# Kernel optimization log

Measured on AMD Instinct MI355X. Metric: run time of the kernel, lower is better.

## Reference

```python
import jax, jax.numpy as jnp
import numpy as np

INPUT_SIZE = 1024
HIDDEN_SIZE = 2048
BATCH = 8192


def setup_inputs() -> dict:
    key = jax.random.key(0)
    k1, k2, k3, k4, k5 = jax.random.split(key, 5)
    input_tensor = jax.random.normal(k1, (BATCH, INPUT_SIZE), dtype=jnp.float32)
    h_0 = jax.random.normal(k2, (BATCH, HIDDEN_SIZE), dtype=jnp.float32)
    c_0 = jax.random.normal(k3, (BATCH, HIDDEN_SIZE), dtype=jnp.float32)
    # parameters: weight [input_size, 3*hidden], weight_hidden [hidden, 3*hidden], bias [3*hidden]
    weight = jax.random.normal(k4, (INPUT_SIZE, 3 * HIDDEN_SIZE), dtype=jnp.float32) * 0.02
    weight_hidden = jax.random.normal(k5, (HIDDEN_SIZE, 3 * HIDDEN_SIZE), dtype=jnp.float32) * 0.02
    bias = jnp.zeros((3 * HIDDEN_SIZE,), dtype=jnp.float32)
    return {
        "input_tensor": input_tensor,
        "h_0": h_0,
        "c_0": c_0,
        "weight": weight,
        "weight_hidden": weight_hidden,
        "bias": bias,
    }


def reference(input_tensor, h_0, c_0, weight, weight_hidden, bias):
    hidden_size = h_0.shape[-1]
    # pre-activations: x @ W + h_0 @ W_h + b  -> [batch, 3*hidden]
    gates = input_tensor @ weight + h_0 @ weight_hidden + bias
    f, i, c = jnp.split(gates, 3, axis=1)
    # c_1 = sigmoid(f) * c_0 + sigmoid(i) * tanh(c)
    c_1 = jax.nn.sigmoid(f) * c_0 + jax.nn.sigmoid(i) * jnp.tanh(c)
    return c_1
```

## Files before the change

### kernel.cpp

```cpp
#include <hip/hip_runtime.h>
#include <stdint.h>


#define BATCH 8192
#define INSZ  1024
#define HID   2048
#define NG    6144
#define KTOT  3072
#define KTILES 96

typedef __attribute__((ext_vector_type(8))) short short8;
typedef __attribute__((ext_vector_type(4))) short short4v;
typedef __attribute__((ext_vector_type(4))) float f32x4;
typedef __attribute__((ext_vector_type(4))) unsigned short u16x4;

__device__ __forceinline__ unsigned short f32_to_bf16(float f) {
  uint32_t u = __builtin_bit_cast(uint32_t, f);
  u += 0x7fffu + ((u >> 16) & 1u);
  return (unsigned short)(u >> 16);
}


__global__ __launch_bounds__(256) void pack_a_kernel(
    const float* __restrict__ x, const float* __restrict__ h,
    unsigned short* __restrict__ Ap) {
  uint32_t q   = blockIdx.x * 256u + threadIdx.x;
  uint32_t kk4 = q & 7u;
  uint32_t m   = (q >> 3) & 8191u;
  uint32_t kt  = q >> 16;
  uint32_t k   = kt * 32u + kk4 * 4u;
  const float* src = (k < INSZ) ? (x + (size_t)m * INSZ + k)
                                : (h + (size_t)m * HID + (k - INSZ));
  float4 v = *(const float4*)src;
  u16x4 o;
  o.x = f32_to_bf16(v.x); o.y = f32_to_bf16(v.y);
  o.z = f32_to_bf16(v.z); o.w = f32_to_bf16(v.w);
  uint32_t c  = kk4 >> 1, hh = kk4 & 1;
  uint32_t sm = (m + (m >> 2)) & 3u;
  *(u16x4*)(Ap + ((size_t)kt * BATCH + m) * 32 + ((c ^ sm) * 8 + hh * 4)) = o;
}

__global__ __launch_bounds__(256) void pack_b_kernel(
    const float* __restrict__ W, const float* __restrict__ Wh,
    unsigned short* __restrict__ Bp) {
  uint32_t q  = blockIdx.x * 256u + threadIdx.x;
  uint32_t hh = q & 7u;
  uint32_t r  = q >> 3;
  uint32_t n  = r % 6144u;
  uint32_t kt = r / 6144u;
  uint32_t k0 = kt * 32u + hh * 4u;
  float v[4];
#pragma unroll
  for (int t = 0; t < 4; ++t) {
    uint32_t k = k0 + t;
    v[t] = (k < INSZ) ? W[(size_t)k * NG + n]
                      : Wh[(size_t)(k - INSZ) * NG + n];
  }
  u16x4 o;
  o.x = f32_to_bf16(v[0]); o.y = f32_to_bf16(v[1]);
  o.z = f32_to_bf16(v[2]); o.w = f32_to_bf16(v[3]);
  *(u16x4*)(Bp + ((size_t)kt * NG + n) * 32 + hh * 4) = o;
}

__device__ __forceinline__ void lstm_epilogue(
    const f32x4 acc[4][6], int m0, int j0, int wm, int wn, int quad, int l16,
    const float* __restrict__ bias, const float* __restrict__ c0,
    float* __restrict__ out) {
#pragma unroll
  for (int mi = 0; mi < 4; ++mi) {
    int rowb = m0 + wm * 64 + mi * 16 + quad * 4;
#pragma unroll
    for (int p = 0; p < 2; ++p) {
      int j = j0 + (2 * wn + p) * 16 + l16;
      float bfv = bias[j], biv = bias[HID + j], bcv = bias[2 * HID + j];
#pragma unroll
      for (int r = 0; r < 4; ++r) {
        size_t idx = (size_t)(rowb + r) * HID + j;
        float fg = acc[mi][0 + p][r] + bfv;
        float ig = acc[mi][2 + p][r] + biv;
        float cg = acc[mi][4 + p][r] + bcv;
        float sf = 1.f / (1.f + __expf(-fg));
        float si = 1.f / (1.f + __expf(-ig));
        float th = 2.f / (1.f + __expf(-2.f * cg)) - 1.f;
        out[idx] = sf * c0[idx] + si * th;
      }
    }
  }
}

__global__ __launch_bounds__(256) void gemm_packed_kernel(
    const unsigned short* __restrict__ Ap, const unsigned short* __restrict__ Bp,
    const float* __restrict__ bias, const float* __restrict__ c0,
    float* __restrict__ out) {
  __shared__ __align__(16) unsigned short As[128 * 32];
  const int tid = threadIdx.x;
  const int lane = tid & 63, w = tid >> 6;
  const int wm = w >> 1, wn = w & 1;
  const int quad = lane >> 4, l16 = lane & 15;
  const int bx = blockIdx.x;
  const int mt = bx & 63, jt = bx >> 6;
  const int m0 = mt * 128, j0 = jt * 64;
  const int sw = (l16 + (l16 >> 2)) & 3;

  f32x4 acc[4][6];
#pragma unroll
  for (int a = 0; a < 4; ++a)
#pragma unroll
    for (int b = 0; b < 6; ++b) acc[a][b] = (f32x4){0.f, 0.f, 0.f, 0.f};

  const unsigned short* bb =
      Bp + ((size_t)(j0 + 2 * wn * 16 + l16)) * 32 + quad * 8;

  short8 bf[2][6];
#pragma unroll
  for (int g = 0; g < 3; ++g)
#pragma unroll
    for (int p = 0; p < 2; ++p)
      bf[0][g * 2 + p] = *(const short8*)(bb + g * (HID * 32) + p * 512);

#pragma unroll 2
  for (int kt = 0; kt < KTILES; ++kt) {
    const int cur = kt & 1;
    const unsigned short* ga = Ap + ((size_t)kt * BATCH + m0) * 32;
#pragma unroll
    for (int i = 0; i < 2; ++i) {
      int t2 = w * 2 + i;
      __builtin_amdgcn_global_load_lds(
          (__attribute__((address_space(1))) void*)(void*)(ga + t2 * 512 + lane * 8),
          (__attribute__((address_space(3))) void*)(As + t2 * 512), 16, 0, 0);
    }
    __syncthreads();
    if (kt + 1 < KTILES) {
      const unsigned short* bn = bb + (size_t)(kt + 1) * (NG * 32);
#pragma unroll
      for (int g = 0; g < 3; ++g)
#pragma unroll
        for (int p = 0; p < 2; ++p)
          bf[cur ^ 1][g * 2 + p] = *(const short8*)(bn + g * (HID * 32) + p * 512);
    }
    short8 af[4];
#pragma unroll
    for (int mi = 0; mi < 4; ++mi)
      af[mi] = *(const short8*)(
          As + (wm * 64 + mi * 16 + l16) * 32 + ((quad ^ sw) * 8));
#pragma unroll
    for (int mi = 0; mi < 4; ++mi)
#pragma unroll
      for (int f = 0; f < 6; ++f)
        acc[mi][f] =
            __builtin_amdgcn_mfma_f32_16x16x32_bf16(af[mi], bf[cur][f], acc[mi][f], 0, 0, 0);
    __syncthreads();
  }
  lstm_epilogue(acc, m0, j0, wm, wn, quad, l16, bias, c0, out);
}

__global__ __launch_bounds__(256) void gemm_f32_kernel(
    const float* __restrict__ x, const float* __restrict__ h,
    const float* __restrict__ W, const float* __restrict__ Wh,
    const float* __restrict__ bias, const float* __restrict__ c0,
    float* __restrict__ out) {
  __shared__ __align__(16) unsigned short As[128 * 36];
  __shared__ __align__(16) unsigned short Bs[192 * 36];
  const int tid = threadIdx.x;
  const int lane = tid & 63, w = tid >> 6;
  const int wm = w >> 1, wn = w & 1;
  const int quad = lane >> 4, l16 = lane & 15;
  const int bx = blockIdx.x;
  const int jt = bx & 31, mt = bx >> 5;
  const int m0 = mt * 128, j0 = jt * 64;

  f32x4 acc[4][6];
#pragma unroll
  for (int a = 0; a < 4; ++a)
#pragma unroll
    for (int b = 0; b < 6; ++b) acc[a][b] = (f32x4){0.f, 0.f, 0.f, 0.f};

  for (int kt = 0; kt < KTILES; ++kt) {
    int k0 = kt * 32;
#pragma unroll
    for (int i = 0; i < 4; ++i) {
      int q = i * 256 + tid;
      int m = q >> 3, kk = (q & 7) * 4;
      int k = k0 + kk;
      const float* src = (k < INSZ) ? (x + (size_t)(m0 + m) * INSZ + k)
                                    : (h + (size_t)(m0 + m) * HID + (k - INSZ));
      float4 v = *(const float4*)src;
      u16x4 o;
      o.x = f32_to_bf16(v.x); o.y = f32_to_bf16(v.y);
      o.z = f32_to_bf16(v.z); o.w = f32_to_bf16(v.w);
      *(u16x4*)(As + m * 36 + kk) = o;
    }
#pragma unroll
    for (int i = 0; i < 6; ++i) {
      int q = i * 256 + tid;
      int n = q % 192, kq = (q / 192) * 4;
      int col = (n >> 6) * HID + j0 + (n & 63);
      float vv[4];
#pragma unroll
      for (int t = 0; t < 4; ++t) {
        int k = k0 + kq + t;
        vv[t] = (k < INSZ) ? W[(size_t)k * NG + col]
                           : Wh[(size_t)(k - INSZ) * NG + col];
      }
      u16x4 o;
      o.x = f32_to_bf16(vv[0]); o.y = f32_to_bf16(vv[1]);
      o.z = f32_to_bf16(vv[2]); o.w = f32_to_bf16(vv[3]);
      *(u16x4*)(Bs + n * 36 + kq) = o;
    }
    __syncthreads();
    short8 af[4], bf[6];
#pragma unroll
    for (int mi = 0; mi < 4; ++mi) {
      int base = (wm * 64 + mi * 16 + l16) * 36 + quad * 8;
      short4v lo = *(const short4v*)(As + base);
      short4v hi = *(const short4v*)(As + base + 4);
      af[mi] = __builtin_shufflevector(lo, hi, 0, 1, 2, 3, 4, 5, 6, 7);
    }
#pragma unroll
    for (int g = 0; g < 3; ++g)
#pragma unroll
      for (int p = 0; p < 2; ++p) {
        int base = (g * 64 + (2 * wn + p) * 16 + l16) * 36 + quad * 8;
        short4v lo = *(const short4v*)(Bs + base);
        short4v hi = *(const short4v*)(Bs + base + 4);
        bf[g * 2 + p] = __builtin_shufflevector(lo, hi, 0, 1, 2, 3, 4, 5, 6, 7);
      }
#pragma unroll
    for (int mi = 0; mi < 4; ++mi)
#pragma unroll
      for (int f = 0; f < 6; ++f)
        acc[mi][f] =
            __builtin_amdgcn_mfma_f32_16x16x32_bf16(af[mi], bf[f], acc[mi][f], 0, 0, 0);
    __syncthreads();
  }
  lstm_epilogue(acc, m0, j0, wm, wn, quad, l16, bias, c0, out);
}

extern "C" void kernel_launch(void* const* d_in, const int* in_sizes, int n_in,
                              void* d_out, int out_size, void* d_ws, size_t ws_size,
                              hipStream_t stream) {
  const float* x    = (const float*)d_in[0];
  const float* h0   = (const float*)d_in[1];
  const float* c0   = (const float*)d_in[2];
  const float* W    = (const float*)d_in[3];
  const float* Wh   = (const float*)d_in[4];
  const float* bias = (const float*)d_in[5];
  float* out = (float*)d_out;

  const size_t needA = (size_t)KTOT * BATCH * 2;
  const size_t needB = (size_t)KTOT * NG * 2;
  if (ws_size >= needA + needB) {
    unsigned short* Ap = (unsigned short*)d_ws;
    unsigned short* Bp = Ap + (size_t)KTOT * BATCH;
    pack_a_kernel<<<24576, 256, 0, stream>>>(x, h0, Ap);
    pack_b_kernel<<<18432, 256, 0, stream>>>(W, Wh, Bp);
    gemm_packed_kernel<<<2048, 256, 0, stream>>>(Ap, Bp, bias, c0, out);
  } else {
    gemm_f32_kernel<<<2048, 256, 0, stream>>>(x, h0, W, Wh, bias, c0, out);
  }
}
```

Measured before the change: 636.0 us.

## Transpose B-pack via shared memory and stream GEMM operands directly from global

Rewrites the weight packing kernel so each block reads coalesced float4 rows into a shared tile and writes the k-packed layout from there, replacing strided scalar loads. The GEMM no longer stages A in LDS with barriers. Each wave loads its A and B fragments straight from global memory each k-tile, with a 2-blocks-per-CU occupancy hint, and the A-pack swizzle is removed to match. This removes synchronisation but leaves global load latency unhidden by explicit prefetch and relies on cache reuse across waves.

```diff
diff --git a/kernel.cpp b/kernel.cpp
--- a/kernel.cpp
+++ b/kernel.cpp
@@ -12,6 +12,7 @@
 typedef __attribute__((ext_vector_type(8))) short short8;
 typedef __attribute__((ext_vector_type(4))) short short4v;
 typedef __attribute__((ext_vector_type(4))) float f32x4;
+typedef __attribute__((ext_vector_type(2))) unsigned short u16x2;
 typedef __attribute__((ext_vector_type(4))) unsigned short u16x4;
 
 __device__ __forceinline__ unsigned short f32_to_bf16(float f) {
@@ -35,31 +36,43 @@
   u16x4 o;
   o.x = f32_to_bf16(v.x); o.y = f32_to_bf16(v.y);
   o.z = f32_to_bf16(v.z); o.w = f32_to_bf16(v.w);
-  uint32_t c  = kk4 >> 1, hh = kk4 & 1;
-  uint32_t sm = (m + (m >> 2)) & 3u;
-  *(u16x4*)(Ap + ((size_t)kt * BATCH + m) * 32 + ((c ^ sm) * 8 + hh * 4)) = o;
+  *(u16x4*)(Ap + ((size_t)kt * BATCH + m) * 32 + kk4 * 4) = o;
 }
 
 __global__ __launch_bounds__(256) void pack_b_kernel(
     const float* __restrict__ W, const float* __restrict__ Wh,
     unsigned short* __restrict__ Bp) {
-  uint32_t q  = blockIdx.x * 256u + threadIdx.x;
-  uint32_t hh = q & 7u;
-  uint32_t r  = q >> 3;
-  uint32_t n  = r % 6144u;
-  uint32_t kt = r / 6144u;
-  uint32_t k0 = kt * 32u + hh * 4u;
-  float v[4];
-#pragma unroll
-  for (int t = 0; t < 4; ++t) {
-    uint32_t k = k0 + t;
-    v[t] = (k < INSZ) ? W[(size_t)k * NG + n]
-                      : Wh[(size_t)(k - INSZ) * NG + n];
-  }
-  u16x4 o;
-  o.x = f32_to_bf16(v[0]); o.y = f32_to_bf16(v[1]);
-  o.z = f32_to_bf16(v[2]); o.w = f32_to_bf16(v[3]);
-  *(u16x4*)(Bp + ((size_t)kt * NG + n) * 32 + hh * 4) = o;
+  __shared__ unsigned short tile[32 * 522];
+  const int tid = threadIdx.x;
+  const int kt = blockIdx.x / 12;
+  const int n0 = (blockIdx.x % 12) * 512;
+  const int k0 = kt * 32;
+  const float* base; int kb;
+  if (k0 < INSZ) { base = W;  kb = k0; }
+  else           { base = Wh; kb = k0 - INSZ; }
+#pragma unroll
+  for (int i = 0; i < 16; ++i) {
+    int t  = i * 256 + tid;
+    int kk = t >> 7, n4 = (t & 127) * 4;
+    float4 v = *(const float4*)(base + (size_t)(kb + kk) * NG + n0 + n4);
+    u16x2 lo, hi;
+    lo.x = f32_to_bf16(v.x); lo.y = f32_to_bf16(v.y);
+    hi.x = f32_to_bf16(v.z); hi.y = f32_to_bf16(v.w);
+    *(u16x2*)(tile + kk * 522 + n4)     = lo;
+    *(u16x2*)(tile + kk * 522 + n4 + 2) = hi;
+  }
+  __syncthreads();
+#pragma unroll
+  for (int i = 0; i < 16; ++i) {
+    int o = i * 256 + tid;
+    int n = o >> 3, u = o & 7;
+    u16x4 val;
+    val.x = tile[(u * 4 + 0) * 522 + n];
+    val.y = tile[(u * 4 + 1) * 522 + n];
+    val.z = tile[(u * 4 + 2) * 522 + n];
+    val.w = tile[(u * 4 + 3) * 522 + n];
+    *(u16x4*)(Bp + ((size_t)kt * NG + n0 + n) * 32 + u * 4) = val;
+  }
 }
 
 __device__ __forceinline__ void lstm_epilogue(
@@ -88,11 +101,10 @@
   }
 }
 
-__global__ __launch_bounds__(256) void gemm_packed_kernel(
+__global__ __launch_bounds__(256, 2) void gemm_stream_kernel(
     const unsigned short* __restrict__ Ap, const unsigned short* __restrict__ Bp,
     const float* __restrict__ bias, const float* __restrict__ c0,
     float* __restrict__ out) {
-  __shared__ __align__(16) unsigned short As[128 * 32];
   const int tid = threadIdx.x;
   const int lane = tid & 63, w = tid >> 6;
   const int wm = w >> 1, wn = w & 1;
@@ -100,7 +112,6 @@
   const int bx = blockIdx.x;
   const int mt = bx & 63, jt = bx >> 6;
   const int m0 = mt * 128, j0 = jt * 64;
-  const int sw = (l16 + (l16 >> 2)) & 3;
 
   f32x4 acc[4][6];
 #pragma unroll
@@ -108,48 +119,28 @@
 #pragma unroll
     for (int b = 0; b < 6; ++b) acc[a][b] = (f32x4){0.f, 0.f, 0.f, 0.f};
 
-  const unsigned short* bb =
-      Bp + ((size_t)(j0 + 2 * wn * 16 + l16)) * 32 + quad * 8;
-
-  short8 bf[2][6];
-#pragma unroll
-  for (int g = 0; g < 3; ++g)
-#pragma unroll
-    for (int p = 0; p < 2; ++p)
-      bf[0][g * 2 + p] = *(const short8*)(bb + g * (HID * 32) + p * 512);
+  const unsigned short* pa = Ap + ((size_t)(m0 + wm * 64 + l16)) * 32 + quad * 8;
+  const unsigned short* pb = Bp + ((size_t)(j0 + 2 * wn * 16 + l16)) * 32 + quad * 8;
 
 #pragma unroll 2
   for (int kt = 0; kt < KTILES; ++kt) {
-    const int cur = kt & 1;
-    const unsigned short* ga = Ap + ((size_t)kt * BATCH + m0) * 32;
-#pragma unroll
-    for (int i = 0; i < 2; ++i) {
-      int t2 = w * 2 + i;
-      __builtin_amdgcn_global_load_lds(
-          (__attribute__((address_space(1))) void*)(void*)(ga + t2 * 512 + lane * 8),
-          (__attribute__((address_space(3))) void*)(As + t2 * 512), 16, 0, 0);
-    }
-    __syncthreads();
-    if (kt + 1 < KTILES) {
-      const unsigned short* bn = bb + (size_t)(kt + 1) * (NG * 32);
-#pragma unroll
-      for (int g = 0; g < 3; ++g)
-#pragma unroll
-        for (int p = 0; p < 2; ++p)
-          bf[cur ^ 1][g * 2 + p] = *(const short8*)(bn + g * (HID * 32) + p * 512);
-    }
-    short8 af[4];
+    short8 af[4], bf[6];
 #pragma unroll
     for (int mi = 0; mi < 4; ++mi)
-      af[mi] = *(const short8*)(
-          As + (wm * 64 + mi * 16 + l16) * 32 + ((quad ^ sw) * 8));
+      af[mi] = *(const short8*)(pa + mi * 512);
+#pragma unroll
+    for (int g = 0; g < 3; ++g)
+#pragma unroll
+      for (int p = 0; p < 2; ++p)
+        bf[g * 2 + p] = *(const short8*)(pb + g * (HID * 32) + p * 512);
 #pragma unroll
     for (int mi = 0; mi < 4; ++mi)
 #pragma unroll
       for (int f = 0; f < 6; ++f)
         acc[mi][f] =
-            __builtin_amdgcn_mfma_f32_16x16x32_bf16(af[mi], bf[cur][f], acc[mi][f], 0, 0, 0);
-    __syncthreads();
+            __builtin_amdgcn_mfma_f32_16x16x32_bf16(af[mi], bf[f], acc[mi][f], 0, 0, 0);
+    pa += (size_t)BATCH * 32;
+    pb += (size_t)NG * 32;
   }
   lstm_epilogue(acc, m0, j0, wm, wn, quad, l16, bias, c0, out);
 }
@@ -253,8 +244,8 @@
     unsigned short* Ap = (unsigned short*)d_ws;
     unsigned short* Bp = Ap + (size_t)KTOT * BATCH;
     pack_a_kernel<<<24576, 256, 0, stream>>>(x, h0, Ap);
-    pack_b_kernel<<<18432, 256, 0, stream>>>(W, Wh, Bp);
-    gemm_packed_kernel<<<2048, 256, 0, stream>>>(Ap, Bp, bias, c0, out);
+    pack_b_kernel<<<1152, 256, 0, stream>>>(W, Wh, Bp);
+    gemm_stream_kernel<<<2048, 256, 0, stream>>>(Ap, Bp, bias, c0, out);
   } else {
     gemm_f32_kernel<<<2048, 256, 0, stream>>>(x, h0, W, Wh, bias, c0, out);
   }
```

New measurement: 689.8 us. 8.5% more time.
